# Optimization experiments

Hardware: AMD Instinct MI355X
Metric: run time of the kernel (lower is better)

Reference implementation:

```python
import jax, jax.numpy as jnp
import numpy as np

N, HID, HEADS = 50000, 256, 8
D = HID // HEADS  # per-head dim = 32
E = 800000


def setup_inputs() -> dict:
    key = jax.random.key(0)
    ks = jax.random.split(key, 12)
    s = 0.02
    x = jax.random.normal(ks[0], (N, HID), dtype=jnp.float32)
    edge_index = jax.random.randint(ks[1], (2, E), 0, N, dtype=jnp.int64)
    # TransformerConv params (PyG defaults: root_weight=True, concat=True, beta=False)
    Wq = jax.random.normal(ks[2], (HID, HID), dtype=jnp.float32) * s
    bq = jnp.zeros((HID,), dtype=jnp.float32)
    Wk = jax.random.normal(ks[3], (HID, HID), dtype=jnp.float32) * s
    bk = jnp.zeros((HID,), dtype=jnp.float32)
    Wv = jax.random.normal(ks[4], (HID, HID), dtype=jnp.float32) * s
    bv = jnp.zeros((HID,), dtype=jnp.float32)
    Wskip = jax.random.normal(ks[5], (HID, HID), dtype=jnp.float32) * s
    bskip = jnp.zeros((HID,), dtype=jnp.float32)
    gamma = jnp.ones((HID,), dtype=jnp.float32)
    beta = jnp.zeros((HID,), dtype=jnp.float32)
    return {"x": x, "edge_index": edge_index, "Wq": Wq, "bq": bq, "Wk": Wk,
            "bk": bk, "Wv": Wv, "bv": bv, "Wskip": Wskip, "bskip": bskip,
            "gamma": gamma, "beta": beta}


def _gnn_layer(x, edge_index, Wq, bq, Wk, bk, Wv, bv, Wskip, bskip, gamma, beta):
    n = x.shape[0]
    src, dst = edge_index[0], edge_index[1]  # messages flow src(j) -> dst(i)
    q = (x @ Wq + bq).reshape(n, HEADS, D)
    k = (x @ Wk + bk).reshape(n, HEADS, D)
    v = (x @ Wv + bv).reshape(n, HEADS, D)
    # per-edge attention logits [E, HEADS]
    logits = jnp.einsum('ehd,ehd->eh', q[dst], k[src]) / jnp.sqrt(jnp.float32(D))
    # segment softmax over destination neighborhoods (stable)
    seg_max = jax.ops.segment_max(logits, dst, num_segments=n)  # [N, HEADS]
    expv = jnp.exp(logits - seg_max[dst])
    denom = jax.ops.segment_sum(expv, dst, num_segments=n)
    attn = expv / denom[dst]  # [E, HEADS]  (dropout in eval mode -> identity)
    # scatter-aggregate weighted values, concat heads
    agg = jax.ops.segment_sum(attn[:, :, None] * v[src], dst, num_segments=n)
    out = agg.reshape(n, HID) + (x @ Wskip + bskip)  # root/skip connection
    h = jax.nn.gelu(out, approximate=False)
    # residual + LayerNorm
    y = x + h
    mu = jnp.mean(y, axis=-1, keepdims=True)
    var = jnp.var(y, axis=-1, keepdims=True)
    return (y - mu) / jnp.sqrt(var + 1e-5) * gamma + beta


def reference(x, edge_index, Wq, bq, Wk, bk, Wv, bv, Wskip, bskip, gamma, beta):
    return _gnn_layer(x, edge_index, Wq, bq, Wk, bk, Wv, bv, Wskip, bskip, gamma, beta)
```

## Files before the change

kernel.cpp:

```cpp
#include <hip/hip_runtime.h>

#define N_NODES 50000
#define HID 256
#define HEADS 8
#define HDIM 32
#define N_EDGES 800000

typedef __bf16 bf16x8 __attribute__((ext_vector_type(8)));
typedef float f32x4 __attribute__((ext_vector_type(4)));
typedef float f32x2 __attribute__((ext_vector_type(2)));

__device__ __forceinline__ unsigned short f2bf(float f) {
    unsigned int b = __float_as_uint(f);
    unsigned int r = (b + 0x7FFFu + ((b >> 16) & 1u)) >> 16;
    return (unsigned short)r;
}
__device__ __forceinline__ float bf2f(unsigned short u) {
    return __uint_as_float(((unsigned int)u) << 16);
}
__device__ __forceinline__ f32x2 bfpair(unsigned int u) {
    f32x2 r;
    r[0] = __uint_as_float(u << 16);
    r[1] = __uint_as_float(u & 0xffff0000u);
    return r;
}

__global__ __launch_bounds__(256) void prep_kernel(
    const float* __restrict__ x, unsigned short* __restrict__ xb,
    const int* __restrict__ dst, int* __restrict__ deg) {
    int b = blockIdx.x;
    if (b < 6250) {
        int t = b * 256 + threadIdx.x;
        const float4* p = reinterpret_cast<const float4*>(x) + (size_t)t * 2;
        float4 f0 = p[0], f1 = p[1];
        uint4 o;
        o.x = (unsigned)f2bf(f0.x) | ((unsigned)f2bf(f0.y) << 16);
        o.y = (unsigned)f2bf(f0.z) | ((unsigned)f2bf(f0.w) << 16);
        o.z = (unsigned)f2bf(f1.x) | ((unsigned)f2bf(f1.y) << 16);
        o.w = (unsigned)f2bf(f1.z) | ((unsigned)f2bf(f1.w) << 16);
        reinterpret_cast<uint4*>(xb)[t] = o;
    } else {
        int e = (b - 6250) * 256 + threadIdx.x;
        atomicAdd(&deg[dst[e]], 1);
    }
}

__device__ __forceinline__ void fused_col_map(int p, int& mat, int& col, float& scale) {
    if (p < 256) { mat = 0; col = p; scale = 1.0f; }
    else if (p < 768) {
        int pp = p - 256;
        mat = ((pp & 2) ? 2 : 1);
        col = ((pp >> 2) << 1) | (pp & 1);
        scale = 64.0f;
    } else { mat = 3; col = p - 768; scale = 1.0f; }
}

__global__ __launch_bounds__(256) void pack_w_kernel(
    const float* __restrict__ Wq, const float* __restrict__ Wk,
    const float* __restrict__ Wv, const float* __restrict__ Ws,
    const float* __restrict__ bq, const float* __restrict__ bk,
    const float* __restrict__ bv, const float* __restrict__ bs,
    unsigned short* __restrict__ wpack, float* __restrict__ biasF) {
    int t = blockIdx.x * 256 + threadIdx.x;
    int e = t & 7, lane = (t >> 3) & 63, kk = (t >> 9) & 7, n_tile = t >> 12;
    int k = kk * 32 + (lane >> 4) * 8 + e;
    int p = n_tile * 16 + (lane & 15);
    const float* W[4] = {Wq, Wk, Wv, Ws};
    int mat, col; float scale;
    fused_col_map(p, mat, col, scale);
    wpack[t] = f2bf(W[mat][k * 256 + col] * scale);
    if (t < 1024) {
        const float* B[4] = {bq, bk, bv, bs};
        int mat2, col2; float s2;
        fused_col_map(t, mat2, col2, s2);
        biasF[t] = B[mat2][col2] * s2;
    }
}

__global__ __launch_bounds__(1024) void scan1_kernel(
    const int* __restrict__ deg, int* __restrict__ row_ptr,
    int* __restrict__ btot, int n) {
    int tid = threadIdx.x, lane = tid & 63, wv = tid >> 6;
    int idx = blockIdx.x * 1024 + tid;
    int v = (idx < n) ? deg[idx] : 0;
    int inc = v;
#pragma unroll
    for (int off = 1; off < 64; off <<= 1) {
        int t2 = __shfl_up(inc, off);
        if (lane >= off) inc += t2;
    }
    __shared__ int sW[16], sO[16];
    if (lane == 63) sW[wv] = inc;
    __syncthreads();
    if (tid < 16) {
        int vv = sW[tid], in2 = vv;
        for (int off = 1; off < 16; off <<= 1) {
            int t2 = __shfl_up(in2, off);
            if (tid >= off) in2 += t2;
        }
        sO[tid] = in2 - vv;
    }
    __syncthreads();
    int excl = sO[wv] + inc - v;
    if (idx <= n) row_ptr[idx] = excl;
    if (tid == 1023) btot[blockIdx.x] = excl + v;
}

__global__ __launch_bounds__(64) void scan2_kernel(
    const int* __restrict__ btot, int* __restrict__ boff, int nb) {
    int t = threadIdx.x;
    int v = (t < nb) ? btot[t] : 0;
    int inc = v;
#pragma unroll
    for (int off = 1; off < 64; off <<= 1) {
        int t2 = __shfl_up(inc, off);
        if (t >= off) inc += t2;
    }
    if (t < nb) boff[t] = inc - v;
}

__global__ __launch_bounds__(256) void fixup_kernel(
    int* __restrict__ row_ptr, int* __restrict__ fill,
    const int* __restrict__ boff, int n) {
    int idx = blockIdx.x * 256 + threadIdx.x;
    if (idx > n) return;
    int v = row_ptr[idx] + boff[idx >> 10];
    row_ptr[idx] = v;
    if (idx < n) fill[idx] = v;
}

__global__ __launch_bounds__(256) void scatter_kernel(
    const int* __restrict__ src, const int* __restrict__ dst,
    int* __restrict__ fill, int* __restrict__ csr_src, int ne) {
    int e = blockIdx.x * 256 + threadIdx.x;
    if (e < ne) {
        int pos = atomicAdd(&fill[dst[e]], 1);
        csr_src[pos] = src[e];
    }
}

__global__ __launch_bounds__(256) void gemm_kernel(
    const unsigned short* __restrict__ xb,
    const unsigned short* __restrict__ wpack,
    const float* __restrict__ biasF,
    unsigned char* __restrict__ qkvs,
    int n_nodes) {
    int bid = blockIdx.x;
    int work = (bid & 7) * 782 + (bid >> 3);
    int mt = work >> 4;
    int nt = work & 15;
    int lane = threadIdx.x & 63;
    int wv = threadIdx.x >> 6;
    int row_w = mt * 128 + wv * 32;
    int n0 = nt * 64;

    f32x4 acc[2][4];
#pragma unroll
    for (int mi = 0; mi < 2; ++mi)
#pragma unroll
        for (int ni = 0; ni < 4; ++ni) {
            f32x4 z = {0.f, 0.f, 0.f, 0.f};
            acc[mi][ni] = z;
        }

    int arow0 = min(row_w + (lane & 15), n_nodes - 1);
    int arow1 = min(row_w + 16 + (lane & 15), n_nodes - 1);
    int acol = (lane >> 4) * 8;
    const uint4* bbase = reinterpret_cast<const uint4*>(wpack);
    int ntile0 = n0 >> 4;

#pragma unroll
    for (int kk = 0; kk < 8; ++kk) {
        bf16x8 a[2], b[4];
        {
            uint4 u0 = *reinterpret_cast<const uint4*>(xb + (size_t)arow0 * 256 + kk * 32 + acol);
            uint4 u1 = *reinterpret_cast<const uint4*>(xb + (size_t)arow1 * 256 + kk * 32 + acol);
            a[0] = __builtin_bit_cast(bf16x8, u0);
            a[1] = __builtin_bit_cast(bf16x8, u1);
        }
#pragma unroll
        for (int ni = 0; ni < 4; ++ni) {
            uint4 u = bbase[((size_t)(ntile0 + ni) * 8 + kk) * 64 + lane];
            b[ni] = __builtin_bit_cast(bf16x8, u);
        }
#pragma unroll
        for (int mi = 0; mi < 2; ++mi)
#pragma unroll
            for (int ni = 0; ni < 4; ++ni)
                acc[mi][ni] = __builtin_amdgcn_mfma_f32_16x16x32_bf16(a[mi], b[ni], acc[mi][ni], 0, 0, 0);
    }

    int region = (n0 < 256) ? 0 : (n0 < 768 ? 1 : 2);
#pragma unroll
    for (int mi = 0; mi < 2; ++mi) {
        int rbase = row_w + mi * 16 + (lane >> 4) * 4;
#pragma unroll
        for (int ni = 0; ni < 4; ++ni) {
            int col = n0 + ni * 16 + (lane & 15);
            float bias = biasF[col];
#pragma unroll
            for (int r = 0; r < 4; ++r) {
                int row = rbase + r;
                if (row < n_nodes) {
                    float val = acc[mi][ni][r] + bias;
                    size_t rb = (size_t)row * 1536;
                    if (region == 0) {
                        *reinterpret_cast<unsigned short*>(qkvs + rb + col * 2) = f2bf(val);
                    } else if (region == 1) {
                        int p8 = __builtin_amdgcn_cvt_pk_fp8_f32(val, val, 0, false);
                        qkvs[rb + 512 + (col - 256)] = (unsigned char)(p8 & 0xff);
                    } else {
                        *reinterpret_cast<unsigned short*>(qkvs + rb + 1024 + (col - 768) * 2) = f2bf(val);
                    }
                }
            }
        }
    }
}

__global__ __launch_bounds__(256) void edge_agg_kernel(
    const int* __restrict__ row_ptr, const int* __restrict__ csr_src,
    const unsigned char* __restrict__ qkvs, const unsigned short* __restrict__ xb,
    const float* __restrict__ gamma, const float* __restrict__ beta,
    float* __restrict__ out) {
    int wv = threadIdx.x >> 6;
    int i = blockIdx.x * 4 + wv;
    int lane = threadIdx.x & 63;
    int half = lane >> 5, l = lane & 31;

    const float QS = 0.17677669529663687f * 1.4426950408889634f / 64.0f;
    const unsigned char* rowi = qkvs + (unsigned)i * 1536u;
    uint4 qu = *reinterpret_cast<const uint4*>(rowi + l * 16);
    f32x2 qsc = {QS, QS};
    f32x2 q01 = bfpair(qu.x) * qsc;
    f32x2 q23 = bfpair(qu.y) * qsc;
    f32x2 q45 = bfpair(qu.z) * qsc;
    f32x2 q67 = bfpair(qu.w) * qsc;

    int e0 = row_ptr[i], e1 = row_ptr[i + 1];
    f32x2 acc0 = {0.f, 0.f}, acc1 = {0.f, 0.f}, acc2 = {0.f, 0.f}, acc3 = {0.f, 0.f};
    float den = 0.f;
    int e = e0 + half;
    int j = (e < e1) ? csr_src[e] : 0;
    while (e < e1) {
        int jn = (e + 2 < e1) ? csr_src[e + 2] : 0;
        uint4 u = *reinterpret_cast<const uint4*>(
            qkvs + (unsigned)j * 1536u + 512u + (unsigned)l * 16u);
        f32x2 k01 = __builtin_amdgcn_cvt_pk_f32_fp8(u.x, false);
        f32x2 v01 = __builtin_amdgcn_cvt_pk_f32_fp8(u.x, true);
        f32x2 k23 = __builtin_amdgcn_cvt_pk_f32_fp8(u.y, false);
        f32x2 v23 = __builtin_amdgcn_cvt_pk_f32_fp8(u.y, true);
        f32x2 k45 = __builtin_amdgcn_cvt_pk_f32_fp8(u.z, false);
        f32x2 v45 = __builtin_amdgcn_cvt_pk_f32_fp8(u.z, true);
        f32x2 k67 = __builtin_amdgcn_cvt_pk_f32_fp8(u.w, false);
        f32x2 v67 = __builtin_amdgcn_cvt_pk_f32_fp8(u.w, true);
        f32x2 d = q01 * k01;
        d = __builtin_elementwise_fma(q23, k23, d);
        d = __builtin_elementwise_fma(q45, k45, d);
        d = __builtin_elementwise_fma(q67, k67, d);
        float s = d[0] + d[1];
        s += __shfl_xor(s, 1);
        s += __shfl_xor(s, 2);
        float w = exp2f(s);
        den += w;
        f32x2 w2 = {w, w};
        acc0 = __builtin_elementwise_fma(w2, v01, acc0);
        acc1 = __builtin_elementwise_fma(w2, v23, acc1);
        acc2 = __builtin_elementwise_fma(w2, v45, acc2);
        acc3 = __builtin_elementwise_fma(w2, v67, acc3);
        j = jn;
        e += 2;
    }

    acc0[0] += __shfl_xor(acc0[0], 32); acc0[1] += __shfl_xor(acc0[1], 32);
    acc1[0] += __shfl_xor(acc1[0], 32); acc1[1] += __shfl_xor(acc1[1], 32);
    acc2[0] += __shfl_xor(acc2[0], 32); acc2[1] += __shfl_xor(acc2[1], 32);
    acc3[0] += __shfl_xor(acc3[0], 32); acc3[1] += __shfl_xor(acc3[1], 32);
    den += __shfl_xor(den, 32);
    float inv = (den > 0.f) ? 1.0f / (den * 64.0f) : 0.f;

    uint4 su = *reinterpret_cast<const uint4*>(rowi + 1024 + l * 16);
    uint4 xu = *reinterpret_cast<const uint4*>(
        reinterpret_cast<const unsigned char*>(xb) + (unsigned)i * 512u + l * 16);
    const float C1 = -2.3022650556f;
    const float C2 = -0.10294578f;
    float s1 = 0.f, s2 = 0.f;
    f32x2 y01, y23, y45, y67;
#define GNN_PROC(A, SRAW, XRAW, Y)                                   \
    {                                                                \
        f32x2 sk = bfpair(SRAW), xr = bfpair(XRAW);                  \
        _Pragma("unroll")                                            \
        for (int qq = 0; qq < 2; ++qq) {                             \
            float pre = fmaf(A[qq], inv, sk[qq]);                    \
            float x2 = pre * pre;                                    \
            float arg = pre * fmaf(C2, x2, C1);                      \
            float gel = pre / (1.f + exp2f(arg));                    \
            float yy = xr[qq] + gel;                                 \
            Y[qq] = yy;                                              \
            s1 += yy;                                                \
            s2 = fmaf(yy, yy, s2);                                   \
        }                                                            \
    }
    GNN_PROC(acc0, su.x, xu.x, y01)
    GNN_PROC(acc1, su.y, xu.y, y23)
    GNN_PROC(acc2, su.z, xu.z, y45)
    GNN_PROC(acc3, su.w, xu.w, y67)
#undef GNN_PROC

#pragma unroll
    for (int m = 1; m <= 16; m <<= 1) {
        s1 += __shfl_xor(s1, m);
        s2 += __shfl_xor(s2, m);
    }
    float mu = s1 * (1.f / 256.f);
    float var = s2 * (1.f / 256.f) - mu * mu;
    float rstd = rsqrtf(var + 1e-5f);

    if (half == 0) {
        const float4* g4 = reinterpret_cast<const float4*>(gamma) + l * 2;
        const float4* b4 = reinterpret_cast<const float4*>(beta) + l * 2;
        float4 ga = g4[0], gb = g4[1], ba = b4[0], bb = b4[1];
        float4 o0, o1;
        o0.x = (y01[0] - mu) * rstd * ga.x + ba.x;
        o0.y = (y01[1] - mu) * rstd * ga.y + ba.y;
        o0.z = (y23[0] - mu) * rstd * ga.z + ba.z;
        o0.w = (y23[1] - mu) * rstd * ga.w + ba.w;
        o1.x = (y45[0] - mu) * rstd * gb.x + bb.x;
        o1.y = (y45[1] - mu) * rstd * gb.y + bb.y;
        o1.z = (y67[0] - mu) * rstd * gb.z + bb.z;
        o1.w = (y67[1] - mu) * rstd * gb.w + bb.w;
        float4* op = reinterpret_cast<float4*>(out + (unsigned)i * 256u + l * 8);
        op[0] = o0;
        op[1] = o1;
    }
}

extern "C" void kernel_launch(void* const* d_in, const int* in_sizes, int n_in,
                              void* d_out, int out_size, void* d_ws, size_t ws_size,
                              hipStream_t stream) {
    const float* x    = (const float*)d_in[0];
    const int*   ei   = (const int*)d_in[1];
    const float* Wq   = (const float*)d_in[2];
    const float* bq   = (const float*)d_in[3];
    const float* Wk   = (const float*)d_in[4];
    const float* bk   = (const float*)d_in[5];
    const float* Wv   = (const float*)d_in[6];
    const float* bv   = (const float*)d_in[7];
    const float* Wsk  = (const float*)d_in[8];
    const float* bsk  = (const float*)d_in[9];
    const float* gamma = (const float*)d_in[10];
    const float* beta  = (const float*)d_in[11];
    const int* src = ei;
    const int* dst = ei + N_EDGES;

    char* ws = (char*)d_ws;
    size_t off = 0;
    auto alloc = [&](size_t bytes) -> void* {
        void* p = ws + off;
        off += (bytes + 255) & ~(size_t)255;
        return p;
    };
    unsigned short* xb     = (unsigned short*)alloc((size_t)N_NODES * 256 * 2);
    unsigned char*  qkvs   = (unsigned char*)alloc((size_t)N_NODES * 1536);
    unsigned short* wpack  = (unsigned short*)alloc(262144 * 2);
    float*          biasF  = (float*)alloc(1024 * 4);
    int*            deg    = (int*)alloc((size_t)N_NODES * 4);
    int*            rowp   = (int*)alloc((size_t)(N_NODES + 1) * 4);
    int*            fill   = (int*)alloc((size_t)N_NODES * 4);
    int*            csr    = (int*)alloc((size_t)N_EDGES * 4);
    int*            btot   = (int*)alloc(64 * 4);
    int*            boff   = (int*)alloc(64 * 4);
    (void)ws_size;

    hipMemsetAsync(deg, 0, (size_t)N_NODES * 4, stream);
    prep_kernel<<<9375, 256, 0, stream>>>(x, xb, dst, deg);
    pack_w_kernel<<<1024, 256, 0, stream>>>(Wq, Wk, Wv, Wsk, bq, bk, bv, bsk, wpack, biasF);
    scan1_kernel<<<50, 1024, 0, stream>>>(deg, rowp, btot, N_NODES);
    scan2_kernel<<<1, 64, 0, stream>>>(btot, boff, 50);
    fixup_kernel<<<196, 256, 0, stream>>>(rowp, fill, boff, N_NODES);
    scatter_kernel<<<3125, 256, 0, stream>>>(src, dst, fill, csr, N_EDGES);
    gemm_kernel<<<6256, 256, 0, stream>>>(xb, wpack, biasF, qkvs, N_NODES);
    edge_agg_kernel<<<12500, 256, 0, stream>>>(rowp, csr, qkvs, xb, gamma, beta, (float*)d_out);
}
```

Before: 265.9 us.

## Fuse weight packing into prep, merge scan kernels, split QKVS buffers, prefetch GEMM

Result: slower. 317.0 us (+19.2%).

```diff
diff --git a/kernel.cpp b/kernel.cpp
--- a/kernel.cpp
+++ b/kernel.cpp
@@ -25,9 +25,24 @@
     return r;
 }
 
+__device__ __forceinline__ void fused_col_map(int p, int& mat, int& col, float& scale) {
+    if (p < 256) { mat = 0; col = p; scale = 1.0f; }
+    else if (p < 768) {
+        int pp = p - 256;
+        mat = ((pp & 2) ? 2 : 1);
+        col = ((pp >> 2) << 1) | (pp & 1);
+        scale = 64.0f;
+    } else { mat = 3; col = p - 768; scale = 1.0f; }
+}
+
 __global__ __launch_bounds__(256) void prep_kernel(
     const float* __restrict__ x, unsigned short* __restrict__ xb,
-    const int* __restrict__ dst, int* __restrict__ deg) {
+    const int* __restrict__ dst, int* __restrict__ deg,
+    const float* __restrict__ Wq, const float* __restrict__ Wk,
+    const float* __restrict__ Wv, const float* __restrict__ Ws,
+    const float* __restrict__ bq, const float* __restrict__ bk,
+    const float* __restrict__ bv, const float* __restrict__ bs,
+    unsigned short* __restrict__ wpack, float* __restrict__ biasF) {
     int b = blockIdx.x;
     if (b < 6250) {
         int t = b * 256 + threadIdx.x;
@@ -39,41 +54,24 @@
         o.z = (unsigned)f2bf(f1.x) | ((unsigned)f2bf(f1.y) << 16);
         o.w = (unsigned)f2bf(f1.z) | ((unsigned)f2bf(f1.w) << 16);
         reinterpret_cast<uint4*>(xb)[t] = o;
-    } else {
+    } else if (b < 9375) {
         int e = (b - 6250) * 256 + threadIdx.x;
         atomicAdd(&deg[dst[e]], 1);
-    }
-}
-
-__device__ __forceinline__ void fused_col_map(int p, int& mat, int& col, float& scale) {
-    if (p < 256) { mat = 0; col = p; scale = 1.0f; }
-    else if (p < 768) {
-        int pp = p - 256;
-        mat = ((pp & 2) ? 2 : 1);
-        col = ((pp >> 2) << 1) | (pp & 1);
-        scale = 64.0f;
-    } else { mat = 3; col = p - 768; scale = 1.0f; }
-}
-
-__global__ __launch_bounds__(256) void pack_w_kernel(
-    const float* __restrict__ Wq, const float* __restrict__ Wk,
-    const float* __restrict__ Wv, const float* __restrict__ Ws,
-    const float* __restrict__ bq, const float* __restrict__ bk,
-    const float* __restrict__ bv, const float* __restrict__ bs,
-    unsigned short* __restrict__ wpack, float* __restrict__ biasF) {
-    int t = blockIdx.x * 256 + threadIdx.x;
-    int e = t & 7, lane = (t >> 3) & 63, kk = (t >> 9) & 7, n_tile = t >> 12;
-    int k = kk * 32 + (lane >> 4) * 8 + e;
-    int p = n_tile * 16 + (lane & 15);
-    const float* W[4] = {Wq, Wk, Wv, Ws};
-    int mat, col; float scale;
-    fused_col_map(p, mat, col, scale);
-    wpack[t] = f2bf(W[mat][k * 256 + col] * scale);
-    if (t < 1024) {
-        const float* B[4] = {bq, bk, bv, bs};
-        int mat2, col2; float s2;
-        fused_col_map(t, mat2, col2, s2);
-        biasF[t] = B[mat2][col2] * s2;
+    } else {
+        int t = (b - 9375) * 256 + threadIdx.x;
+        int e = t & 7, lane = (t >> 3) & 63, kk = (t >> 9) & 7, n_tile = t >> 12;
+        int k = kk * 32 + (lane >> 4) * 8 + e;
+        int p = n_tile * 16 + (lane & 15);
+        const float* W[4] = {Wq, Wk, Wv, Ws};
+        int mat, col; float scale;
+        fused_col_map(p, mat, col, scale);
+        wpack[t] = f2bf(W[mat][k * 256 + col] * scale);
+        if (t < 1024) {
+            const float* B[4] = {bq, bk, bv, bs};
+            int mat2, col2; float s2;
+            fused_col_map(t, mat2, col2, s2);
+            biasF[t] = B[mat2][col2] * s2;
+        }
     }
 }
 
@@ -106,25 +104,25 @@
     if (tid == 1023) btot[blockIdx.x] = excl + v;
 }
 
-__global__ __launch_bounds__(64) void scan2_kernel(
-    const int* __restrict__ btot, int* __restrict__ boff, int nb) {
-    int t = threadIdx.x;
-    int v = (t < nb) ? btot[t] : 0;
-    int inc = v;
-#pragma unroll
-    for (int off = 1; off < 64; off <<= 1) {
-        int t2 = __shfl_up(inc, off);
-        if (t >= off) inc += t2;
-    }
-    if (t < nb) boff[t] = inc - v;
-}
-
 __global__ __launch_bounds__(256) void fixup_kernel(
     int* __restrict__ row_ptr, int* __restrict__ fill,
-    const int* __restrict__ boff, int n) {
-    int idx = blockIdx.x * 256 + threadIdx.x;
+    const int* __restrict__ btot, int n) {
+    __shared__ int sB;
+    int tid = threadIdx.x;
+    if (tid < 64) {
+        int v = (tid < 50) ? btot[tid] : 0;
+        int inc = v;
+#pragma unroll
+        for (int off = 1; off < 64; off <<= 1) {
+            int t2 = __shfl_up(inc, off);
+            if (tid >= off) inc += t2;
+        }
+        if (tid == (blockIdx.x >> 2)) sB = inc - v;
+    }
+    __syncthreads();
+    int idx = blockIdx.x * 256 + tid;
     if (idx > n) return;
-    int v = row_ptr[idx] + boff[idx >> 10];
+    int v = row_ptr[idx] + sB;
     row_ptr[idx] = v;
     if (idx < n) fill[idx] = v;
 }
@@ -143,7 +141,9 @@
     const unsigned short* __restrict__ xb,
     const unsigned short* __restrict__ wpack,
     const float* __restrict__ biasF,
-    unsigned char* __restrict__ qkvs,
+    unsigned short* __restrict__ qs,
+    unsigned char* __restrict__ kv,
+    unsigned short* __restrict__ sk,
     int n_nodes) {
     int bid = blockIdx.x;
     int work = (bid & 7) * 782 + (bid >> 3);
@@ -169,28 +169,37 @@
     const uint4* bbase = reinterpret_cast<const uint4*>(wpack);
     int ntile0 = n0 >> 4;
 
+    uint4 af[2][2], bf[2][4];
+#define LDA(BUF, KK)                                                            \
+    af[BUF][0] = *reinterpret_cast<const uint4*>(                               \
+        xb + (size_t)arow0 * 256 + (KK) * 32 + acol);                           \
+    af[BUF][1] = *reinterpret_cast<const uint4*>(                               \
+        xb + (size_t)arow1 * 256 + (KK) * 32 + acol);
+#define LDB(BUF, KK)                                                            \
+    _Pragma("unroll") for (int ni = 0; ni < 4; ++ni)                            \
+        bf[BUF][ni] = bbase[((size_t)(ntile0 + ni) * 8 + (KK)) * 64 + lane];
+
+    LDA(0, 0)
+    LDB(0, 0)
+
 #pragma unroll
     for (int kk = 0; kk < 8; ++kk) {
-        bf16x8 a[2], b[4];
-        {
-            uint4 u0 = *reinterpret_cast<const uint4*>(xb + (size_t)arow0 * 256 + kk * 32 + acol);
-            uint4 u1 = *reinterpret_cast<const uint4*>(xb + (size_t)arow1 * 256 + kk * 32 + acol);
-            a[0] = __builtin_bit_cast(bf16x8, u0);
-            a[1] = __builtin_bit_cast(bf16x8, u1);
-        }
-#pragma unroll
-        for (int ni = 0; ni < 4; ++ni) {
-            uint4 u = bbase[((size_t)(ntile0 + ni) * 8 + kk) * 64 + lane];
-            b[ni] = __builtin_bit_cast(bf16x8, u);
+        const int buf = kk & 1, nb = buf ^ 1;
+        if (kk < 7) {
+            LDA(nb, kk + 1)
+            LDB(nb, kk + 1)
         }
 #pragma unroll
         for (int mi = 0; mi < 2; ++mi)
 #pragma unroll
             for (int ni = 0; ni < 4; ++ni)
-                acc[mi][ni] = __builtin_amdgcn_mfma_f32_16x16x32_bf16(a[mi], b[ni], acc[mi][ni], 0, 0, 0);
-    }
-
-    int region = (n0 < 256) ? 0 : (n0 < 768 ? 1 : 2);
+                acc[mi][ni] = __builtin_amdgcn_mfma_f32_16x16x32_bf16(
+                    __builtin_bit_cast(bf16x8, af[buf][mi]),
+                    __builtin_bit_cast(bf16x8, bf[buf][ni]), acc[mi][ni], 0, 0, 0);
+    }
+#undef LDA
+#undef LDB
+
 #pragma unroll
     for (int mi = 0; mi < 2; ++mi) {
         int rbase = row_w + mi * 16 + (lane >> 4) * 4;
@@ -203,14 +212,17 @@
                 int row = rbase + r;
                 if (row < n_nodes) {
                     float val = acc[mi][ni][r] + bias;
-                    size_t rb = (size_t)row * 1536;
-                    if (region == 0) {
-                        *reinterpret_cast<unsigned short*>(qkvs + rb + col * 2) = f2bf(val);
-                    } else if (region == 1) {
-                        int p8 = __builtin_amdgcn_cvt_pk_fp8_f32(val, val, 0, false);
-                        qkvs[rb + 512 + (col - 256)] = (unsigned char)(p8 & 0xff);
+                    if (nt < 4) {
+                        __builtin_nontemporal_store(
+                            f2bf(val), qs + (size_t)row * 256 + col);
+                    } else if (nt < 12) {
+                        int d8 = __builtin_amdgcn_cvt_pk_fp8_f32(val, val, 0, false);
+                        __builtin_nontemporal_store(
+                            (unsigned char)(d8 & 0xff),
+                            kv + (size_t)row * 512 + (col - 256));
                     } else {
-                        *reinterpret_cast<unsigned short*>(qkvs + rb + 1024 + (col - 768) * 2) = f2bf(val);
+                        __builtin_nontemporal_store(
+                            f2bf(val), sk + (size_t)row * 256 + (col - 768));
                     }
                 }
             }
@@ -220,7 +232,8 @@
 
 __global__ __launch_bounds__(256) void edge_agg_kernel(
     const int* __restrict__ row_ptr, const int* __restrict__ csr_src,
-    const unsigned char* __restrict__ qkvs, const unsigned short* __restrict__ xb,
+    const unsigned short* __restrict__ qs, const unsigned char* __restrict__ kv,
+    const unsigned short* __restrict__ sk, const unsigned short* __restrict__ xb,
     const float* __restrict__ gamma, const float* __restrict__ beta,
     float* __restrict__ out) {
     int wv = threadIdx.x >> 6;
@@ -229,8 +242,7 @@
     int half = lane >> 5, l = lane & 31;
 
     const float QS = 0.17677669529663687f * 1.4426950408889634f / 64.0f;
-    const unsigned char* rowi = qkvs + (unsigned)i * 1536u;
-    uint4 qu = *reinterpret_cast<const uint4*>(rowi + l * 16);
+    uint4 qu = *reinterpret_cast<const uint4*>(qs + (size_t)i * 256 + l * 8);
     f32x2 qsc = {QS, QS};
     f32x2 q01 = bfpair(qu.x) * qsc;
     f32x2 q23 = bfpair(qu.y) * qsc;
@@ -245,7 +257,7 @@
     while (e < e1) {
         int jn = (e + 2 < e1) ? csr_src[e + 2] : 0;
         uint4 u = *reinterpret_cast<const uint4*>(
-            qkvs + (unsigned)j * 1536u + 512u + (unsigned)l * 16u);
+            kv + (size_t)j * 512u + (unsigned)l * 16u);
         f32x2 k01 = __builtin_amdgcn_cvt_pk_f32_fp8(u.x, false);
         f32x2 v01 = __builtin_amdgcn_cvt_pk_f32_fp8(u.x, true);
         f32x2 k23 = __builtin_amdgcn_cvt_pk_f32_fp8(u.y, false);
@@ -279,19 +291,18 @@
     den += __shfl_xor(den, 32);
     float inv = (den > 0.f) ? 1.0f / (den * 64.0f) : 0.f;
 
-    uint4 su = *reinterpret_cast<const uint4*>(rowi + 1024 + l * 16);
-    uint4 xu = *reinterpret_cast<const uint4*>(
-        reinterpret_cast<const unsigned char*>(xb) + (unsigned)i * 512u + l * 16);
+    uint4 su = *reinterpret_cast<const uint4*>(sk + (size_t)i * 256 + l * 8);
+    uint4 xu = *reinterpret_cast<const uint4*>(xb + (size_t)i * 256 + l * 8);
     const float C1 = -2.3022650556f;
     const float C2 = -0.10294578f;
     float s1 = 0.f, s2 = 0.f;
     f32x2 y01, y23, y45, y67;
 #define GNN_PROC(A, SRAW, XRAW, Y)                                   \
     {                                                                \
-        f32x2 sk = bfpair(SRAW), xr = bfpair(XRAW);                  \
+        f32x2 skp = bfpair(SRAW), xr = bfpair(XRAW);                 \
         _Pragma("unroll")                                            \
         for (int qq = 0; qq < 2; ++qq) {                             \
-            float pre = fmaf(A[qq], inv, sk[qq]);                    \
+            float pre = fmaf(A[qq], inv, skp[qq]);                   \
             float x2 = pre * pre;                                    \
             float arg = pre * fmaf(C2, x2, C1);                      \
             float gel = pre / (1.f + exp2f(arg));                    \
@@ -320,18 +331,18 @@
         const float4* g4 = reinterpret_cast<const float4*>(gamma) + l * 2;
         const float4* b4 = reinterpret_cast<const float4*>(beta) + l * 2;
         float4 ga = g4[0], gb = g4[1], ba = b4[0], bb = b4[1];
-        float4 o0, o1;
-        o0.x = (y01[0] - mu) * rstd * ga.x + ba.x;
-        o0.y = (y01[1] - mu) * rstd * ga.y + ba.y;
-        o0.z = (y23[0] - mu) * rstd * ga.z + ba.z;
-        o0.w = (y23[1] - mu) * rstd * ga.w + ba.w;
-        o1.x = (y45[0] - mu) * rstd * gb.x + bb.x;
-        o1.y = (y45[1] - mu) * rstd * gb.y + bb.y;
-        o1.z = (y67[0] - mu) * rstd * gb.z + bb.z;
-        o1.w = (y67[1] - mu) * rstd * gb.w + bb.w;
-        float4* op = reinterpret_cast<float4*>(out + (unsigned)i * 256u + l * 8);
-        op[0] = o0;
-        op[1] = o1;
+        f32x4 o0, o1;
+        o0[0] = (y01[0] - mu) * rstd * ga.x + ba.x;
+        o0[1] = (y01[1] - mu) * rstd * ga.y + ba.y;
+        o0[2] = (y23[0] - mu) * rstd * ga.z + ba.z;
+        o0[3] = (y23[1] - mu) * rstd * ga.w + ba.w;
+        o1[0] = (y45[0] - mu) * rstd * gb.x + bb.x;
+        o1[1] = (y45[1] - mu) * rstd * gb.y + bb.y;
+        o1[2] = (y67[0] - mu) * rstd * gb.z + bb.z;
+        o1[3] = (y67[1] - mu) * rstd * gb.w + bb.w;
+        f32x4* op = reinterpret_cast<f32x4*>(out + (size_t)i * 256 + l * 8);
+        __builtin_nontemporal_store(o0, op);
+        __builtin_nontemporal_store(o1, op + 1);
     }
 }
 
@@ -361,7 +372,9 @@
         return p;
     };
     unsigned short* xb     = (unsigned short*)alloc((size_t)N_NODES * 256 * 2);
-    unsigned char*  qkvs   = (unsigned char*)alloc((size_t)N_NODES * 1536);
+    unsigned short* qs     = (unsigned short*)alloc((size_t)N_NODES * 256 * 2);
+    unsigned char*  kvb    = (unsigned char*)alloc((size_t)N_NODES * 512);
+    unsigned short* sk     = (unsigned short*)alloc((size_t)N_NODES * 256 * 2);
     unsigned short* wpack  = (unsigned short*)alloc(262144 * 2);
     float*          biasF  = (float*)alloc(1024 * 4);
     int*            deg    = (int*)alloc((size_t)N_NODES * 4);
@@ -369,16 +382,15 @@
     int*            fill   = (int*)alloc((size_t)N_NODES * 4);
     int*            csr    = (int*)alloc((size_t)N_EDGES * 4);
     int*            btot   = (int*)alloc(64 * 4);
-    int*            boff   = (int*)alloc(64 * 4);
     (void)ws_size;
 
     hipMemsetAsync(deg, 0, (size_t)N_NODES * 4, stream);
-    prep_kernel<<<9375, 256, 0, stream>>>(x, xb, dst, deg);
-    pack_w_kernel<<<1024, 256, 0, stream>>>(Wq, Wk, Wv, Wsk, bq, bk, bv, bsk, wpack, biasF);
+    prep_kernel<<<10399, 256, 0, stream>>>(x, xb, dst, deg, Wq, Wk, Wv, Wsk,
+                                           bq, bk, bv, bsk, wpack, biasF);
     scan1_kernel<<<50, 1024, 0, stream>>>(deg, rowp, btot, N_NODES);
-    scan2_kernel<<<1, 64, 0, stream>>>(btot, boff, 50);
-    fixup_kernel<<<196, 256, 0, stream>>>(rowp, fill, boff, N_NODES);
+    fixup_kernel<<<196, 256, 0, stream>>>(rowp, fill, btot, N_NODES);
     scatter_kernel<<<3125, 256, 0, stream>>>(src, dst, fill, csr, N_EDGES);
-    gemm_kernel<<<6256, 256, 0, stream>>>(xb, wpack, biasF, qkvs, N_NODES);
-    edge_agg_kernel<<<12500, 256, 0, stream>>>(rowp, csr, qkvs, xb, gamma, beta, (float*)d_out);
-}
+    gemm_kernel<<<6256, 256, 0, stream>>>(xb, wpack, biasF, qs, kvb, sk, N_NODES);
+    edge_agg_kernel<<<12500, 256, 0, stream>>>(rowp, csr, qs, kvb, sk, xb, gamma, beta,
+                                               (float*)d_out);
+}
```
